# Performance work log

Hardware: AMD Instinct MI355X
Metric: run time of the kernel (lower is better)

Reference implementation:

```python
import jax, jax.numpy as jnp
import numpy as np


def _nn_idx(query, ref):
    """Index of nearest ref point for each query point.
    query: [B,N,3], ref: [B,M,3] -> idx [B,N] (int32).
    Squared distance via ||q||^2 - 2 q.r + ||r||^2 (matches cdist+top1).
    """
    d2 = (jnp.sum(query * query, axis=-1, keepdims=True)
          - 2.0 * jnp.einsum('bnd,bmd->bnm', query, ref)
          + jnp.sum(ref * ref, axis=-1)[:, None, :])
    return jnp.argmin(d2, axis=-1)


def setup_inputs() -> dict:
    key = jax.random.key(0)
    k1, k2, k3 = jax.random.split(key, 3)
    B, N, M = 1, 16384, 16384  # batch hard-coded to 1 in original loops
    pred = jax.random.normal(k1, (B, N, 3), dtype=jnp.float32)
    gt = jax.random.normal(k2, (B, M, 3), dtype=jnp.float32)
    weight = jax.random.uniform(k3, (1,), dtype=jnp.float32)
    return {"pred": pred, "gt": gt, "weight": weight}


def reference(pred, gt, weight):
    # get_mse_loss2: weighted bidirectional nearest-neighbor MSE.
    w = weight[0]
    # B2A: align each pred point to its nearest gt point
    idx = _nn_idx(pred, gt)                                   # [B,N]
    align_gt = jnp.take_along_axis(gt, idx[..., None], axis=1)  # [B,N,3]
    B2A = jnp.mean((pred - align_gt) ** 2)
    # A2B: align each gt point to its nearest pred point
    idx2 = _nn_idx(gt, pred)                                  # [B,M]
    align_out = jnp.take_along_axis(pred, idx2[..., None], axis=1)  # [B,M,3]
    A2B = jnp.mean((align_out - gt) ** 2)
    return B2A * w + A2B * (1.0 - w)
```

## Files before the change

### kernel.cpp

```cpp
#include <hip/hip_runtime.h>


#define NPTS   16384
#define QT     2
#define QBLK   (4 * QT * 32)
#define QCH    (NPTS / QBLK)
#define SSPLIT 16
#define RBLK   (NPTS / SSPLIT)
#define NB1    (2 * QCH * SSPLIT)

typedef __attribute__((ext_vector_type(8)))  __bf16 bf16x8;
typedef __attribute__((ext_vector_type(16))) float  floatx16;

union frag16 { __bf16 v[16]; uint4 q[2]; };

__device__ __forceinline__ float vmin16(floatx16 v) {
    float a = fminf(fminf(v[0], v[1]), v[2]);
    float b = fminf(fminf(v[3], v[4]), v[5]);
    float c = fminf(fminf(v[6], v[7]), v[8]);
    float d = fminf(fminf(v[9], v[10]), v[11]);
    float e = fminf(fminf(v[12], v[13]), fminf(v[14], v[15]));
    return fminf(fminf(fminf(a, b), fminf(c, d)), e);
}

__global__ __launch_bounds__(256) void nn_part_kernel(
    const float* __restrict__ pred, const float* __restrict__ gt,
    float* __restrict__ partial)
{
    const int bx   = blockIdx.x;
    const int dir  = bx >> 10;
    const int qc   = (bx & 1023) >> 4;
    const int s    = bx & 15;
    const int tid  = threadIdx.x;
    const int lane = tid & 63;
    const int wave = tid >> 6;
    const int lid  = lane & 31;
    const int half = lane >> 5;

    const float* __restrict__ Q = dir ? gt : pred;
    const float* __restrict__ R = dir ? pred : gt;

    __shared__ uint4 ldsA[RBLK * 2];

    const int rbase = s * RBLK;
    for (int j = tid; j < RBLK; j += 256) {
        const float x = R[(rbase + j) * 3 + 0];
        const float y = R[(rbase + j) * 3 + 1];
        const float z = R[(rbase + j) * 3 + 2];
        const float rr = x * x + y * y + z * z;
        const __bf16 xh = (__bf16)x, yh = (__bf16)y, zh = (__bf16)z;
        const __bf16 xl = (__bf16)(x - (float)xh);
        const __bf16 yl = (__bf16)(y - (float)yh);
        const __bf16 zl = (__bf16)(z - (float)zh);
        const __bf16 rh = (__bf16)rr;
        const __bf16 rl = (__bf16)(rr - (float)rh);
        const __bf16 one = (__bf16)1.0f;
        frag16 A;
        A.v[0]  = (__bf16)(-2.0f * (float)xh); A.v[1]  = A.v[0];
        A.v[2]  = (__bf16)(-2.0f * (float)xl); A.v[3]  = A.v[2];
        A.v[4]  = (__bf16)(-2.0f * (float)yh); A.v[5]  = A.v[4];
        A.v[6]  = (__bf16)(-2.0f * (float)yl); A.v[7]  = A.v[6];
        A.v[8]  = (__bf16)(-2.0f * (float)zh); A.v[9]  = A.v[8];
        A.v[10] = (__bf16)(-2.0f * (float)zl); A.v[11] = A.v[10];
        A.v[12] = rh;  A.v[13] = rl;  A.v[14] = one;  A.v[15] = one;
        const int tile = j >> 5, l = j & 31;
        ldsA[tile * 64 + l]      = A.q[0];
        ldsA[tile * 64 + 32 + l] = A.q[1];
    }

    const int qbase = qc * QBLK + wave * (QT * 32);
    bf16x8 bq[QT];
#pragma unroll
    for (int qt = 0; qt < QT; ++qt) {
        const int p = qbase + qt * 32 + lid;
        const float x = Q[p * 3 + 0], y = Q[p * 3 + 1], z = Q[p * 3 + 2];
        const float qq = x * x + y * y + z * z;
        const __bf16 xh = (__bf16)x, yh = (__bf16)y, zh = (__bf16)z;
        const __bf16 xl = (__bf16)(x - (float)xh);
        const __bf16 yl = (__bf16)(y - (float)yh);
        const __bf16 zl = (__bf16)(z - (float)zh);
        const __bf16 qh = (__bf16)qq;
        const __bf16 ql = (__bf16)(qq - (float)qh);
        const __bf16 one = (__bf16)1.0f;
        frag16 B;
        B.v[0] = xh;  B.v[1]  = xl;  B.v[2]  = xh;  B.v[3]  = xl;
        B.v[4] = yh;  B.v[5]  = yl;  B.v[6]  = yh;  B.v[7]  = yl;
        B.v[8] = zh;  B.v[9]  = zl;  B.v[10] = zh;  B.v[11] = zl;
        B.v[12] = one; B.v[13] = one; B.v[14] = qh;  B.v[15] = ql;
        bq[qt] = __builtin_bit_cast(bf16x8, B.q[half]);
    }

    floatx16 zero;
#pragma unroll
    for (int k = 0; k < 16; ++k) zero[k] = 0.0f;
    floatx16 mnv[QT];
#pragma unroll
    for (int qt = 0; qt < QT; ++qt)
#pragma unroll
        for (int k = 0; k < 16; ++k) mnv[qt][k] = 3.4e38f;

    __syncthreads();

#pragma unroll 2
    for (int t = 0; t < RBLK / 32; t += 2) {
        const bf16x8 a0 = __builtin_bit_cast(bf16x8, ldsA[t * 64 + half * 32 + lid]);
        const bf16x8 a1 = __builtin_bit_cast(bf16x8, ldsA[(t + 1) * 64 + half * 32 + lid]);
#pragma unroll
        for (int qt = 0; qt < QT; ++qt) {
            floatx16 d0 = __builtin_amdgcn_mfma_f32_32x32x16_bf16(a0, bq[qt], zero, 0, 0, 0);
            floatx16 d1 = __builtin_amdgcn_mfma_f32_32x32x16_bf16(a1, bq[qt], zero, 0, 0, 0);
#pragma unroll
            for (int k = 0; k < 16; ++k)
                mnv[qt][k] = fminf(fminf(mnv[qt][k], d0[k]), d1[k]);
        }
    }

    float* pout = partial + ((size_t)((dir * QCH + qc) * SSPLIT + s)) * QBLK
                + wave * (QT * 32);
#pragma unroll
    for (int qt = 0; qt < QT; ++qt) {
        float v = vmin16(mnv[qt]);
        v = fminf(v, __shfl_xor(v, 32));
        if (half == 0) pout[qt * 32 + lid] = v;
    }
}

__global__ __launch_bounds__(256) void nn_combine_kernel(
    const float* __restrict__ partial, const float* __restrict__ weight,
    float* __restrict__ out)
{
    const int b   = blockIdx.x;
    const int dir = b >> 6;
    const int qc  = b & 63;
    const int t   = threadIdx.x;

    const float* p = partial + ((size_t)((dir * QCH + qc) * SSPLIT)) * QBLK;
    float v = p[t];
#pragma unroll
    for (int s = 1; s < SSPLIT; ++s)
        v = fminf(v, p[s * QBLK + t]);

    for (int off = 32; off; off >>= 1) v += __shfl_down(v, off);
    __shared__ float ws[4];
    if ((t & 63) == 0) ws[t >> 6] = v;
    __syncthreads();
    if (t == 0) {
        const float sum = ws[0] + ws[1] + ws[2] + ws[3];
        const float wgt = weight[0];
        const float scale = (dir ? (1.0f - wgt) : wgt) / (3.0f * (float)NPTS);
        atomicAdd(out, sum * scale);
    }
}

extern "C" void kernel_launch(void* const* d_in, const int* in_sizes, int n_in,
                              void* d_out, int out_size, void* d_ws, size_t ws_size,
                              hipStream_t stream) {
    const float* pred   = (const float*)d_in[0];
    const float* gt     = (const float*)d_in[1];
    const float* weight = (const float*)d_in[2];
    float* partial = (float*)d_ws;

    hipMemsetAsync(d_out, 0, sizeof(float), stream);
    nn_part_kernel<<<NB1, 256, 0, stream>>>(pred, gt, partial);
    nn_combine_kernel<<<2 * QCH, 256, 0, stream>>>(partial, weight, (float*)d_out);
}
```

Baseline: 87.66 us.

## Precompute bf16 MFMA fragments in a prep kernel and DMA them into LDS

Adds a prep kernel that converts each point once into the split-bf16 A and B MFMA fragment layouts and writes them to workspace. The main kernel then fills LDS with global_load_lds direct copies and reads query fragments straight from memory. Previously every one of the 2048 blocks redid this conversion for its 1024 reference points. The prep kernel also zeroes the output, replacing the memset call. The cost is an extra kernel launch and writing then reading the fragment buffers through global memory.

```diff
diff --git a/kernel.cpp b/kernel.cpp
--- a/kernel.cpp
+++ b/kernel.cpp
@@ -23,8 +23,59 @@
     return fminf(fminf(fminf(a, b), fminf(c, d)), e);
 }
 
+__device__ __forceinline__ void load_lds16(const uint4* g, uint4* l) {
+    __builtin_amdgcn_global_load_lds(
+        (const __attribute__((address_space(1))) void*)g,
+        (__attribute__((address_space(3))) void*)l, 16, 0, 0);
+}
+
+__global__ __launch_bounds__(256) void prep_kernel(
+    const float* __restrict__ pred, const float* __restrict__ gt,
+    uint4* __restrict__ aform, uint4* __restrict__ bform,
+    float* __restrict__ out)
+{
+    const int i = blockIdx.x * 256 + threadIdx.x;
+    if (i == 0) out[0] = 0.0f;
+    const int role = (i < NPTS) ? 0 : 1;
+    const int p = i - role * NPTS;
+    const float* __restrict__ src = role ? gt : pred;
+
+    const float x = src[p * 3 + 0], y = src[p * 3 + 1], z = src[p * 3 + 2];
+    const float nn = x * x + y * y + z * z;
+    const __bf16 xh = (__bf16)x, yh = (__bf16)y, zh = (__bf16)z;
+    const __bf16 xl = (__bf16)(x - (float)xh);
+    const __bf16 yl = (__bf16)(y - (float)yh);
+    const __bf16 zl = (__bf16)(z - (float)zh);
+    const __bf16 nh = (__bf16)nn;
+    const __bf16 nl = (__bf16)(nn - (float)nh);
+    const __bf16 one = (__bf16)1.0f;
+
+    frag16 A;
+    A.v[0]  = (__bf16)(-2.0f * (float)xh); A.v[1]  = A.v[0];
+    A.v[2]  = (__bf16)(-2.0f * (float)xl); A.v[3]  = A.v[2];
+    A.v[4]  = (__bf16)(-2.0f * (float)yh); A.v[5]  = A.v[4];
+    A.v[6]  = (__bf16)(-2.0f * (float)yl); A.v[7]  = A.v[6];
+    A.v[8]  = (__bf16)(-2.0f * (float)zh); A.v[9]  = A.v[8];
+    A.v[10] = (__bf16)(-2.0f * (float)zl); A.v[11] = A.v[10];
+    A.v[12] = nh;  A.v[13] = nl;  A.v[14] = one;  A.v[15] = one;
+
+    frag16 B;
+    B.v[0] = xh;  B.v[1]  = xl;  B.v[2]  = xh;  B.v[3]  = xl;
+    B.v[4] = yh;  B.v[5]  = yl;  B.v[6]  = yh;  B.v[7]  = yl;
+    B.v[8] = zh;  B.v[9]  = zl;  B.v[10] = zh;  B.v[11] = zl;
+    B.v[12] = one; B.v[13] = one; B.v[14] = nh;  B.v[15] = nl;
+
+    uint4* da = aform + (size_t)role * (NPTS * 2)
+              + ((p >> 5) * 64 + (p & 31));
+    da[0]  = A.q[0];
+    da[32] = A.q[1];
+    uint4* db = bform + (size_t)role * (NPTS * 2) + p * 2;
+    db[0] = B.q[0];
+    db[1] = B.q[1];
+}
+
 __global__ __launch_bounds__(256) void nn_part_kernel(
-    const float* __restrict__ pred, const float* __restrict__ gt,
+    const uint4* __restrict__ aform, const uint4* __restrict__ bform,
     float* __restrict__ partial)
 {
     const int bx   = blockIdx.x;
@@ -37,35 +88,16 @@
     const int lid  = lane & 31;
     const int half = lane >> 5;
 
-    const float* __restrict__ Q = dir ? gt : pred;
-    const float* __restrict__ R = dir ? pred : gt;
+    const uint4* __restrict__ Aref = aform + (size_t)(dir ? 0 : 1) * (NPTS * 2);
+    const uint4* __restrict__ Bqry = bform + (size_t)(dir ? 1 : 0) * (NPTS * 2);
 
     __shared__ uint4 ldsA[RBLK * 2];
 
-    const int rbase = s * RBLK;
-    for (int j = tid; j < RBLK; j += 256) {
-        const float x = R[(rbase + j) * 3 + 0];
-        const float y = R[(rbase + j) * 3 + 1];
-        const float z = R[(rbase + j) * 3 + 2];
-        const float rr = x * x + y * y + z * z;
-        const __bf16 xh = (__bf16)x, yh = (__bf16)y, zh = (__bf16)z;
-        const __bf16 xl = (__bf16)(x - (float)xh);
-        const __bf16 yl = (__bf16)(y - (float)yh);
-        const __bf16 zl = (__bf16)(z - (float)zh);
-        const __bf16 rh = (__bf16)rr;
-        const __bf16 rl = (__bf16)(rr - (float)rh);
-        const __bf16 one = (__bf16)1.0f;
-        frag16 A;
-        A.v[0]  = (__bf16)(-2.0f * (float)xh); A.v[1]  = A.v[0];
-        A.v[2]  = (__bf16)(-2.0f * (float)xl); A.v[3]  = A.v[2];
-        A.v[4]  = (__bf16)(-2.0f * (float)yh); A.v[5]  = A.v[4];
-        A.v[6]  = (__bf16)(-2.0f * (float)yl); A.v[7]  = A.v[6];
-        A.v[8]  = (__bf16)(-2.0f * (float)zh); A.v[9]  = A.v[8];
-        A.v[10] = (__bf16)(-2.0f * (float)zl); A.v[11] = A.v[10];
-        A.v[12] = rh;  A.v[13] = rl;  A.v[14] = one;  A.v[15] = one;
-        const int tile = j >> 5, l = j & 31;
-        ldsA[tile * 64 + l]      = A.q[0];
-        ldsA[tile * 64 + 32 + l] = A.q[1];
+    const uint4* gsrc = Aref + (size_t)s * (RBLK * 2);
+#pragma unroll
+    for (int i = 0; i < 8; ++i) {
+        const int idx = i * 256 + wave * 64;
+        load_lds16(gsrc + idx + lane, &ldsA[idx]);
     }
 
     const int qbase = qc * QBLK + wave * (QT * 32);
@@ -73,21 +105,7 @@
 #pragma unroll
     for (int qt = 0; qt < QT; ++qt) {
         const int p = qbase + qt * 32 + lid;
-        const float x = Q[p * 3 + 0], y = Q[p * 3 + 1], z = Q[p * 3 + 2];
-        const float qq = x * x + y * y + z * z;
-        const __bf16 xh = (__bf16)x, yh = (__bf16)y, zh = (__bf16)z;
-        const __bf16 xl = (__bf16)(x - (float)xh);
-        const __bf16 yl = (__bf16)(y - (float)yh);
-        const __bf16 zl = (__bf16)(z - (float)zh);
-        const __bf16 qh = (__bf16)qq;
-        const __bf16 ql = (__bf16)(qq - (float)qh);
-        const __bf16 one = (__bf16)1.0f;
-        frag16 B;
-        B.v[0] = xh;  B.v[1]  = xl;  B.v[2]  = xh;  B.v[3]  = xl;
-        B.v[4] = yh;  B.v[5]  = yl;  B.v[6]  = yh;  B.v[7]  = yl;
-        B.v[8] = zh;  B.v[9]  = zl;  B.v[10] = zh;  B.v[11] = zl;
-        B.v[12] = one; B.v[13] = one; B.v[14] = qh;  B.v[15] = ql;
-        bq[qt] = __builtin_bit_cast(bf16x8, B.q[half]);
+        bq[qt] = __builtin_bit_cast(bf16x8, Bqry[p * 2 + half]);
     }
 
     floatx16 zero;
@@ -158,9 +176,13 @@
     const float* pred   = (const float*)d_in[0];
     const float* gt     = (const float*)d_in[1];
     const float* weight = (const float*)d_in[2];
+
     float* partial = (float*)d_ws;
+    uint4* aform = (uint4*)((char*)d_ws + (size_t)2 * QCH * SSPLIT * QBLK * 4);
+    uint4* bform = aform + (size_t)2 * NPTS * 2;
 
-    hipMemsetAsync(d_out, 0, sizeof(float), stream);
-    nn_part_kernel<<<NB1, 256, 0, stream>>>(pred, gt, partial);
+    prep_kernel<<<2 * NPTS / 256, 256, 0, stream>>>(pred, gt, aform, bform,
+                                                    (float*)d_out);
+    nn_part_kernel<<<NB1, 256, 0, stream>>>(aform, bform, partial);
     nn_combine_kernel<<<2 * QCH, 256, 0, stream>>>(partial, weight, (float*)d_out);
 }
```

Result: no change. 86.39 us (-1.4%).
